# Kernel tuning notes

Measured on AMD Instinct MI355X. Metric: run time of the kernel, lower is better.

## Reference

```python
import jax, jax.numpy as jnp
import numpy as np

T, KBLK, EMB, B = 2048, 64, 512, 4


def _make_coords(t, k):
    # head1: for each j, cols = block_start(j) + arange(j % k + 1)  (block-causal local)
    j = np.arange(t)
    cnt1 = (j % k) + 1
    rows1 = np.repeat(j, cnt1)
    off1 = np.arange(cnt1.sum()) - np.repeat(np.cumsum(cnt1) - cnt1, cnt1)
    cols1 = (rows1 // k) * k + off1
    # head2: for each block start c, rows = arange(c, t), col = c  (strided block-start)
    starts = np.arange(t // k) * k
    cnt2 = t - starts
    base = np.repeat(starts, cnt2)
    off2 = np.arange(cnt2.sum()) - np.repeat(np.cumsum(cnt2) - cnt2, cnt2)
    rows2, cols2 = base + off2, base
    c1 = np.stack([rows1, cols1], 1).astype(np.int32)
    c2 = np.stack([rows2, cols2], 1).astype(np.int32)
    return c1, c2


def setup_inputs() -> dict:
    key = jax.random.key(0)
    ks = jax.random.split(key, 6)
    s = 1.0 / float(np.sqrt(EMB))
    c1, c2 = _make_coords(T, KBLK)
    return {
        "x": jax.random.normal(ks[0], (B, T, EMB), jnp.float32),
        "Wk": jax.random.normal(ks[1], (EMB, EMB), jnp.float32) * s,
        "bk": jnp.zeros((EMB,), jnp.float32),
        "Wq": jax.random.normal(ks[2], (EMB, EMB), jnp.float32) * s,
        "bq": jnp.zeros((EMB,), jnp.float32),
        "Wv": jax.random.normal(ks[3], (EMB, EMB), jnp.float32) * s,
        "bv": jnp.zeros((EMB,), jnp.float32),
        "Wu": jax.random.normal(ks[4], (EMB, 2 * EMB), jnp.float32) * s,
        "bu": jnp.zeros((EMB,), jnp.float32),
        "coords1": jnp.asarray(c1),
        "coords2": jnp.asarray(c2),
    }


def _sparse_head(Kt, Qt, Vt, coords):
    rows, cols = coords[:, 0], coords[:, 1]
    # dot[b,p] = (K @ Q^T)[b, rows[p], cols[p]] = K[b,rows[p],:] . Q[b,cols[p],:]
    dot = jnp.einsum('bpe,bpe->bp', Kt[:, rows], Qt[:, cols])
    # sparse.batchmm: out[b,r] = sum_{p: rows[p]=r} dot[b,p] * V[b, cols[p]]
    out = jnp.zeros_like(Vt).at[:, rows].add(dot[..., None] * Vt[:, cols])
    return out


def reference(x, Wk, bk, Wq, bq, Wv, bv, Wu, bu, coords1, coords2):
    Kt = x @ Wk.T + bk
    Qt = x @ Wq.T + bq
    Vt = x @ Wv.T + bv
    h1 = _sparse_head(Kt, Qt, Vt, coords1)
    h2 = _sparse_head(Kt, Qt, Vt, coords2)
    comb = jnp.concatenate([h1, h2], axis=-1)  # [B, T, 2*EMB]
    return comb @ Wu.T + bu
```

## Files before the change

### kernel.cpp

```cpp
#include <hip/hip_runtime.h>


typedef unsigned short u16;
typedef __attribute__((ext_vector_type(8))) short short8;
typedef __attribute__((ext_vector_type(4))) float f32x4;

constexpr int TDIM  = 2048;
constexpr int EMB_D = 512;
constexpr int BB    = 4;
constexpr int NBLK  = 32;
constexpr int LDK   = 2048;

__device__ __forceinline__ u16 f2b(float f) {
    unsigned u = __float_as_uint(f);
    unsigned r = (u + 0x7FFFu + ((u >> 16) & 1u)) >> 16;
    return (u16)r;
}

__global__ __launch_bounds__(256) void prep_k(
    const float* __restrict__ x, const float* __restrict__ Wk, const float* __restrict__ Wq,
    const float* __restrict__ Wv, const float* __restrict__ Wu,
    const float* __restrict__ bk, const float* __restrict__ bq, const float* __restrict__ bv,
    u16* __restrict__ xb, u16* __restrict__ wcat, float* __restrict__ biascat)
{
    const int bid = blockIdx.x, tid = threadIdx.x;
    if (bid < 32) {
        const int bm = (bid >> 2) * 128;
        const int bn = (bid & 3) * 128;
        const int wid  = tid >> 6;
        const int lane = tid & 63;
        const int l15  = lane & 15;
        const int quad = lane >> 4;
        const int wm = (wid & 1) * 64;
        const int wn = (wid >> 1) * 64;

        f32x4 acc[4][4] = {};

        const float* Arow[4];
        #pragma unroll
        for (int i = 0; i < 4; ++i) {
            const int m = bm + wm + 16 * i + l15;
            Arow[i] = Wu + (size_t)(m & 511) * 1024 + (m >> 9) * 512 + quad * 8;
        }
        const float* Bcol[4];
        #pragma unroll
        for (int g = 0; g < 4; ++g)
            Bcol[g] = Wv + (bn + wn + 16 * g + l15) + (size_t)(quad * 8) * 512;

        for (int j0 = 0; j0 < 512; j0 += 32) {
            short8 a[4], b[4];
            #pragma unroll
            for (int i = 0; i < 4; ++i) {
                float4 v0 = *(const float4*)(Arow[i] + j0);
                float4 v1 = *(const float4*)(Arow[i] + j0 + 4);
                a[i] = (short8){(short)f2b(v0.x), (short)f2b(v0.y), (short)f2b(v0.z), (short)f2b(v0.w),
                                (short)f2b(v1.x), (short)f2b(v1.y), (short)f2b(v1.z), (short)f2b(v1.w)};
            }
            #pragma unroll
            for (int g = 0; g < 4; ++g) {
                const float* p = Bcol[g] + (size_t)j0 * 512;
                float v0 = p[0];          float v1 = p[512];
                float v2 = p[1024];       float v3 = p[1536];
                float v4 = p[2048];       float v5 = p[2560];
                float v6 = p[3072];       float v7 = p[3584];
                b[g] = (short8){(short)f2b(v0), (short)f2b(v1), (short)f2b(v2), (short)f2b(v3),
                                (short)f2b(v4), (short)f2b(v5), (short)f2b(v6), (short)f2b(v7)};
            }
            #pragma unroll
            for (int i = 0; i < 4; ++i)
                #pragma unroll
                for (int g = 0; g < 4; ++g)
                    acc[i][g] = __builtin_amdgcn_mfma_f32_16x16x32_bf16(a[i], b[g], acc[i][g], 0, 0, 0);
        }

        #pragma unroll
        for (int i = 0; i < 4; ++i)
            #pragma unroll
            for (int g = 0; g < 4; ++g) {
                const int col = bn + wn + 16 * g + l15;
                #pragma unroll
                for (int r = 0; r < 4; ++r) {
                    const int row = bm + wm + 16 * i + quad * 4 + r;
                    wcat[(size_t)(1024 + row) * 512 + col] = f2b(acc[i][g][r]);
                }
            }
    } else if (bid < 4640) {
        const float* src; u16* dst; int base;
        if (bid < 4128)      { src = x;  dst = xb;            base = (bid - 32) * 1024; }
        else if (bid < 4384) { src = Wk; dst = wcat;          base = (bid - 4128) * 1024; }
        else                 { src = Wq; dst = wcat + 262144; base = (bid - 4384) * 1024; }
        const int idx = base + tid * 4;
        float4 v = *(const float4*)(src + idx);
        ushort4 o = { f2b(v.x), f2b(v.y), f2b(v.z), f2b(v.w) };
        *(ushort4*)(dst + idx) = o;
    } else if (bid < 4656) {
        const int o = (bid - 4640) * 64 + (tid >> 2);
        const int p = tid & 3;
        const int n = o & 511, half = o >> 9;
        const float* wr = Wu + (size_t)n * 1024 + half * 512 + p * 128;
        const float* br = bv + p * 128;
        float s = 0.f;
        #pragma unroll
        for (int j = 0; j < 128; j += 4) {
            float4 a = *(const float4*)(wr + j);
            float4 b = *(const float4*)(br + j);
            s += a.x*b.x + a.y*b.y + a.z*b.z + a.w*b.w;
        }
        s += __shfl_xor(s, 1);
        s += __shfl_xor(s, 2);
        if (p == 0) biascat[1024 + o] = s;
    } else {
        const int idx = tid * 4;
        float4 v = (idx < 512) ? *(const float4*)(bk + idx)
                               : *(const float4*)(bq + idx - 512);
        *(float4*)(biascat + idx) = v;
    }
}

template<int MH, int KK>
__device__ __forceinline__ void mm16(const short8 (&a)[4], const short8 (&b)[2][4],
                                     f32x4 (&acc)[8][4])
{
    #pragma unroll
    for (int f = 0; f < 4; ++f)
        #pragma unroll
        for (int g = 0; g < 4; ++g)
            acc[MH * 4 + f][g] = __builtin_amdgcn_mfma_f32_16x16x32_bf16(
                a[f], b[KK][g], acc[MH * 4 + f][g], 0, 0, 0);
}

template<int SLOT, int MH>
__device__ __forceinline__ void lda4(short8 (&a)[4], const u16* sm, int arow, int koff)
{
    #pragma unroll
    for (int f = 0; f < 4; ++f)
        a[f] = *(const short8*)(sm + SLOT * 32768 + (arow + MH * 64 + f * 16) * 64 + koff);
}

template<int SLOT>
__device__ __forceinline__ void ldb4(short8 (&bk)[4], const u16* sm, int brow, int koff)
{
    #pragma unroll
    for (int g = 0; g < 4; ++g)
        bk[g] = *(const short8*)(sm + SLOT * 32768 + 16384 + (brow + g * 16) * 64 + koff);
}

#define STA(S, CI, T) __builtin_amdgcn_global_load_lds( \
    (const __attribute__((address_space(1))) void*)(Ag + (size_t)(CI) * 32768 + (T) * 64), \
    (__attribute__((address_space(3))) void*)(sm + (S) * 32768 + (CI) * 4096 + wid * 512), 16, 0, 0)
#define STB(S, CI, T) __builtin_amdgcn_global_load_lds( \
    (const __attribute__((address_space(1))) void*)(Bg + (size_t)(CI) * 32768 + (T) * 64), \
    (__attribute__((address_space(3))) void*)(sm + (S) * 32768 + 16384 + (CI) * 4096 + wid * 512), 16, 0, 0)
#define KBAR()  __builtin_amdgcn_s_barrier()
#define KPRIO(P) __builtin_amdgcn_s_setprio(P)
#define LGKM0() do { asm volatile("s_waitcnt lgkmcnt(0)" ::: "memory"); \
                     __builtin_amdgcn_sched_barrier(0); } while (0)
#define VMC4()  asm volatile("s_waitcnt vmcnt(4)" ::: "memory")
#define VMC0()  asm volatile("s_waitcnt vmcnt(0)" ::: "memory")

__global__ __launch_bounds__(512, 2) void kqv_gemm_k(
    const u16* __restrict__ A, const u16* __restrict__ W,
    const float* __restrict__ bias, u16* __restrict__ C)
{
    __shared__ u16 sm[65536];

    const int bid = blockIdx.x;
    const int wg  = (bid & 7) * 32 + (bid >> 3);
    const int bm  = (wg & 31) * 256;
    const int bn  = (wg >> 5) * 256;
    const int tid  = threadIdx.x;
    const int wid  = tid >> 6;
    const int lane = tid & 63;
    const int l15  = lane & 15;
    const int quad = lane >> 4;
    const int wm = wid >> 2;
    const int wn = wid & 3;

    const int stgrow = wid * 8 + (lane >> 3);
    const int stgk   = ((lane & 7) ^ ((lane >> 3) & 7)) << 3;
    const u16* Ag = A + (size_t)(bm + stgrow) * 512 + stgk;
    const u16* Bg = W + (size_t)(bn + stgrow) * 512 + stgk;

    const int r7     = l15 & 7;
    const int arow   = wm * 128 + l15;
    const int brow   = wn * 64 + l15;
    const int off_k0 = ((quad ^ r7) << 3);
    const int off_k1 = (((4 | quad) ^ r7) << 3);

    f32x4 acc[8][4] = {};
    short8 a[4], b[2][4];

    STA(0,0,0); STA(0,2,0); STB(0,0,0); STB(0,1,0);
    STB(0,2,0); STB(0,3,0); STA(0,1,0); STA(0,3,0);
    STA(1,0,1); STA(1,2,1); STB(1,0,1); STB(1,1,1);
    VMC4(); KBAR();

    for (int it = 0; it < 3; ++it) {
        const int t = 2 * it;
        ldb4<0>(b[0], sm, brow, off_k0); lda4<0,0>(a, sm, arow, off_k0);
        STB(1,2,t+1); STB(1,3,t+1);
        KBAR(); LGKM0(); KPRIO(1); mm16<0,0>(a, b, acc); KPRIO(0); KBAR();
        ldb4<0>(b[1], sm, brow, off_k1); lda4<0,0>(a, sm, arow, off_k1);
        STA(1,1,t+1); STA(1,3,t+1);
        KBAR(); LGKM0(); KPRIO(1); mm16<0,1>(a, b, acc); KPRIO(0); KBAR();
        lda4<0,1>(a, sm, arow, off_k0);
        STA(0,0,t+2); STA(0,2,t+2);
        KBAR(); LGKM0(); KPRIO(1); mm16<1,0>(a, b, acc); KPRIO(0); KBAR();
        lda4<0,1>(a, sm, arow, off_k1);
        STB(0,0,t+2); STB(0,1,t+2);
        KBAR(); LGKM0(); KPRIO(1); mm16<1,1>(a, b, acc); KPRIO(0); VMC4(); KBAR();
        ldb4<1>(b[0], sm, brow, off_k0); lda4<1,0>(a, sm, arow, off_k0);
        STB(0,2,t+2); STB(0,3,t+2);
        KBAR(); LGKM0(); KPRIO(1); mm16<0,0>(a, b, acc); KPRIO(0); KBAR();
        ldb4<1>(b[1], sm, brow, off_k1); lda4<1,0>(a, sm, arow, off_k1);
        STA(0,1,t+2); STA(0,3,t+2);
        KBAR(); LGKM0(); KPRIO(1); mm16<0,1>(a, b, acc); KPRIO(0); KBAR();
        lda4<1,1>(a, sm, arow, off_k0);
        STA(1,0,t+3); STA(1,2,t+3);
        KBAR(); LGKM0(); KPRIO(1); mm16<1,0>(a, b, acc); KPRIO(0); KBAR();
        lda4<1,1>(a, sm, arow, off_k1);
        STB(1,0,t+3); STB(1,1,t+3);
        KBAR(); LGKM0(); KPRIO(1); mm16<1,1>(a, b, acc); KPRIO(0); VMC4(); KBAR();
    }

    ldb4<0>(b[0], sm, brow, off_k0); lda4<0,0>(a, sm, arow, off_k0);
    STB(1,2,7); STB(1,3,7);
    KBAR(); LGKM0(); KPRIO(1); mm16<0,0>(a, b, acc); KPRIO(0); KBAR();
    ldb4<0>(b[1], sm, brow, off_k1); lda4<0,0>(a, sm, arow, off_k1);
    STA(1,1,7); STA(1,3,7);
    KBAR(); LGKM0(); KPRIO(1); mm16<0,1>(a, b, acc); KPRIO(0); KBAR();
    lda4<0,1>(a, sm, arow, off_k0);
    KBAR(); LGKM0(); KPRIO(1); mm16<1,0>(a, b, acc); KPRIO(0); KBAR();
    lda4<0,1>(a, sm, arow, off_k1);
    KBAR(); LGKM0(); KPRIO(1); mm16<1,1>(a, b, acc); KPRIO(0); VMC0(); KBAR();
    ldb4<1>(b[0], sm, brow, off_k0); lda4<1,0>(a, sm, arow, off_k0);
    KBAR(); LGKM0(); KPRIO(1); mm16<0,0>(a, b, acc); KPRIO(0); KBAR();
    ldb4<1>(b[1], sm, brow, off_k1); lda4<1,0>(a, sm, arow, off_k1);
    KBAR(); LGKM0(); KPRIO(1); mm16<0,1>(a, b, acc); KPRIO(0); KBAR();
    lda4<1,1>(a, sm, arow, off_k0);
    KBAR(); LGKM0(); KPRIO(1); mm16<1,0>(a, b, acc); KPRIO(0); KBAR();
    lda4<1,1>(a, sm, arow, off_k1);
    KBAR(); LGKM0(); KPRIO(1); mm16<1,1>(a, b, acc); KPRIO(0);

    __syncthreads();
    #pragma unroll
    for (int mf = 0; mf < 8; ++mf) {
        #pragma unroll
        for (int g = 0; g < 4; ++g) {
            const int col = wn * 64 + g * 16 + l15;
            const float bvv = bias[bn + col];
            #pragma unroll
            for (int r = 0; r < 4; ++r) {
                const int row = wm * 128 + mf * 16 + quad * 4 + r;
                sm[row * 256 + col] = f2b(acc[mf][g][r] + bvv);
            }
        }
    }
    __syncthreads();
    {
        const int rr = tid >> 5;
        const int ck = tid & 31;
        #pragma unroll
        for (int p = 0; p < 16; ++p) {
            const int row = p * 16 + rr;
            short8 v = *(const short8*)(sm + row * 256 + ck * 8);
            *(short8*)(C + (size_t)(bm + row) * LDK + bn + ck * 8) = v;
        }
    }
}

#undef STA
#undef STB
#undef KBAR
#undef KPRIO
#undef LGKM0
#undef VMC4
#undef VMC0

__global__ __launch_bounds__(512) void heads_k(
    const u16* __restrict__ KQV, const float* __restrict__ bu, float* __restrict__ out)
{
    __shared__ u16 smA[64 * 104];
    __shared__ u16 smVT[256 * 104];
    __shared__ u16 pK[2][64 * 32];
    __shared__ u16 pQ[2][64 * 32];
    __shared__ u16 pQs[2][32 * 32];

    const int blk = blockIdx.x, b = blockIdx.y;
    const int e0 = blockIdx.z * 256;
    const int tid = threadIdx.x;
    const int wid = tid >> 6, lane = tid & 63;
    const int l15 = lane & 15, quad = lane >> 4;
    const int rw = wid & 3, ch = wid >> 2;
    const size_t row0 = (size_t)b * TDIM + (size_t)blk * 64;
    const size_t brow = (size_t)b * TDIM;
    const int srow_base = 16 * rw + quad * 4;

    #pragma unroll
    for (int it = 0; it < 4; ++it) {
        const int id = tid + 512 * it;
        const int c  = id & 63;
        const int eo = (id >> 6) * 8;
        short8 v = *(const short8*)(KQV + (row0 + c) * (size_t)LDK + 1024 + e0 + eo);
        #pragma unroll
        for (int i = 0; i < 8; ++i) smVT[(eo + i) * 104 + c] = (u16)v[i];
    }
    #pragma unroll
    for (int it = 0; it < 2; ++it) {
        const int id = tid + 512 * it;
        const int m  = id & 31;
        const int eo = (id >> 5) * 8;
        short8 v = *(const short8*)(KQV + (brow + 64 * m) * (size_t)LDK + 1536 + e0 + eo);
        #pragma unroll
        for (int i = 0; i < 8; ++i) smVT[(eo + i) * 104 + 64 + m] = (u16)v[i];
    }

    f32x4 s1[2] = {}; f32x4 s2 = {};
    const int strow  = (tid >> 2) & 63;
    const int sthalf = tid >> 8;
    const int stk    = (tid & 3) * 8;
    const u16* Kg = KQV + (row0 + strow) * (size_t)LDK + sthalf * 32 + stk;
    const u16* Qg = Kg + 512;
    const int qrow  = (tid >> 2) & 31;
    const int qhalf = (tid >> 7) & 1;
    const u16* Qsg = KQV + (brow + (size_t)64 * qrow) * (size_t)LDK + 512 + qhalf * 32 + stk;
    char* dK  = (char*)pK  + wid * 1024;
    char* dQ  = (char*)pQ  + wid * 1024;
    char* dQs = (char*)pQs + wid * 1024;

    for (int k0 = 0; k0 < 512; k0 += 64) {
        __syncthreads();
        __builtin_amdgcn_global_load_lds(
            (const __attribute__((address_space(1))) void*)(Kg + k0),
            (__attribute__((address_space(3))) void*)dK, 16, 0, 0);
        __builtin_amdgcn_global_load_lds(
            (const __attribute__((address_space(1))) void*)(Qg + k0),
            (__attribute__((address_space(3))) void*)dQ, 16, 0, 0);
        if (wid < 4)
            __builtin_amdgcn_global_load_lds(
                (const __attribute__((address_space(1))) void*)(Qsg + k0),
                (__attribute__((address_space(3))) void*)dQs, 16, 0, 0);
        __syncthreads();

        short8 a0 = *(const short8*)(pK[0] + (16 * rw + l15) * 32 + quad * 8);
        short8 a1 = *(const short8*)(pK[1] + (16 * rw + l15) * 32 + quad * 8);
        #pragma unroll
        for (int jj = 0; jj < 2; ++jj) {
            const int j = 2 * ch + jj;
            short8 b0 = *(const short8*)(pQ[0] + (16 * j + l15) * 32 + quad * 8);
            short8 b1 = *(const short8*)(pQ[1] + (16 * j + l15) * 32 + quad * 8);
            s1[jj] = __builtin_amdgcn_mfma_f32_16x16x32_bf16(a0, b0, s1[jj], 0, 0, 0);
            s1[jj] = __builtin_amdgcn_mfma_f32_16x16x32_bf16(a1, b1, s1[jj], 0, 0, 0);
        }
        {
            short8 b0 = *(const short8*)(pQs[0] + (16 * ch + l15) * 32 + quad * 8);
            short8 b1 = *(const short8*)(pQs[1] + (16 * ch + l15) * 32 + quad * 8);
            s2 = __builtin_amdgcn_mfma_f32_16x16x32_bf16(a0, b0, s2, 0, 0, 0);
            s2 = __builtin_amdgcn_mfma_f32_16x16x32_bf16(a1, b1, s2, 0, 0, 0);
        }
    }

    #pragma unroll
    for (int jj = 0; jj < 2; ++jj)
        #pragma unroll
        for (int r = 0; r < 4; ++r) {
            const int rr = srow_base + r;
            const int cc = 32 * ch + 16 * jj + l15;
            smA[rr * 104 + cc] = f2b((cc <= rr) ? s1[jj][r] : 0.0f);
        }
    #pragma unroll
    for (int r = 0; r < 4; ++r) {
        const int m  = 16 * ch + l15;
        const int rr = srow_base + r;
        smA[rr * 104 + 64 + m] = f2b((m <= blk) ? s2[r] : 0.0f);
    }
    __syncthreads();

    f32x4 o[8] = {};
    const u16* arow = smA + (16 * rw + l15) * 104;
    #pragma unroll
    for (int ks = 0; ks < 3; ++ks) {
        short8 as = *(const short8*)(arow + 32 * ks + quad * 8);
        #pragma unroll
        for (int nt = 0; nt < 8; ++nt) {
            short8 bs = *(const short8*)(smVT + (16 * (8 * ch + nt) + l15) * 104 + 32 * ks + quad * 8);
            o[nt] = __builtin_amdgcn_mfma_f32_16x16x32_bf16(as, bs, o[nt], 0, 0, 0);
        }
    }
    #pragma unroll
    for (int nt = 0; nt < 8; ++nt) {
        const int col = e0 + 16 * (8 * ch + nt) + l15;
        const float bvv = bu[col];
        #pragma unroll
        for (int r = 0; r < 4; ++r)
            out[(row0 + srow_base + r) * (size_t)EMB_D + col] = o[nt][r] + bvv;
    }
}

extern "C" void kernel_launch(void* const* d_in, const int* in_sizes, int n_in,
                              void* d_out, int out_size, void* d_ws, size_t ws_size,
                              hipStream_t stream)
{
    const float* x  = (const float*)d_in[0];
    const float* Wk = (const float*)d_in[1];
    const float* bk = (const float*)d_in[2];
    const float* Wq = (const float*)d_in[3];
    const float* bq = (const float*)d_in[4];
    const float* Wv = (const float*)d_in[5];
    const float* bv = (const float*)d_in[6];
    const float* Wu = (const float*)d_in[7];
    const float* bu = (const float*)d_in[8];
    float* out = (float*)d_out;

    char* w = (char*)d_ws;
    u16*   KQV     = (u16*)  (w + ((size_t)0  << 20));
    u16*   xb      = (u16*)  (w + ((size_t)32 << 20));
    u16*   wcat    = (u16*)  (w + ((size_t)40 << 20));
    float* biascat = (float*)(w + ((size_t)44 << 20));

    hipLaunchKernelGGL(prep_k, dim3(4657), dim3(256), 0, stream,
                       x, Wk, Wq, Wv, Wu, bk, bq, bv, xb, wcat, biascat);
    hipLaunchKernelGGL(kqv_gemm_k, dim3(256), dim3(512), 0, stream, xb, wcat, biascat, KQV);
    hipLaunchKernelGGL(heads_k, dim3(NBLK, BB, 2), dim3(512), 0, stream, KQV, bu, out);
}
```

Baseline: 141.5 us.

## Replace pipelined 256x256 GEMM with simple single-buffered 128x256 tiles at higher occupancy

The hand-scheduled, double-buffered 256x256 KQV GEMM with setprio and manual waitcnts is replaced by a plain loop over 128x256 tiles. Each iteration loads one K-slice into LDS and syncs twice, and the grid doubles to 512 blocks. The smaller LDS footprint and accumulator set allow more blocks per CU, and the epilogue now writes bf16 directly to global memory instead of staging through LDS. The cost is the loss of load/compute overlap and more B-matrix traffic. The scattered 2-byte global stores may also hurt coalescing.

```diff
diff --git a/kernel.cpp b/kernel.cpp
--- a/kernel.cpp
+++ b/kernel.cpp
@@ -117,57 +117,15 @@
     }
 }
 
-template<int MH, int KK>
-__device__ __forceinline__ void mm16(const short8 (&a)[4], const short8 (&b)[2][4],
-                                     f32x4 (&acc)[8][4])
-{
-    #pragma unroll
-    for (int f = 0; f < 4; ++f)
-        #pragma unroll
-        for (int g = 0; g < 4; ++g)
-            acc[MH * 4 + f][g] = __builtin_amdgcn_mfma_f32_16x16x32_bf16(
-                a[f], b[KK][g], acc[MH * 4 + f][g], 0, 0, 0);
-}
-
-template<int SLOT, int MH>
-__device__ __forceinline__ void lda4(short8 (&a)[4], const u16* sm, int arow, int koff)
-{
-    #pragma unroll
-    for (int f = 0; f < 4; ++f)
-        a[f] = *(const short8*)(sm + SLOT * 32768 + (arow + MH * 64 + f * 16) * 64 + koff);
-}
-
-template<int SLOT>
-__device__ __forceinline__ void ldb4(short8 (&bk)[4], const u16* sm, int brow, int koff)
-{
-    #pragma unroll
-    for (int g = 0; g < 4; ++g)
-        bk[g] = *(const short8*)(sm + SLOT * 32768 + 16384 + (brow + g * 16) * 64 + koff);
-}
-
-#define STA(S, CI, T) __builtin_amdgcn_global_load_lds( \
-    (const __attribute__((address_space(1))) void*)(Ag + (size_t)(CI) * 32768 + (T) * 64), \
-    (__attribute__((address_space(3))) void*)(sm + (S) * 32768 + (CI) * 4096 + wid * 512), 16, 0, 0)
-#define STB(S, CI, T) __builtin_amdgcn_global_load_lds( \
-    (const __attribute__((address_space(1))) void*)(Bg + (size_t)(CI) * 32768 + (T) * 64), \
-    (__attribute__((address_space(3))) void*)(sm + (S) * 32768 + 16384 + (CI) * 4096 + wid * 512), 16, 0, 0)
-#define KBAR()  __builtin_amdgcn_s_barrier()
-#define KPRIO(P) __builtin_amdgcn_s_setprio(P)
-#define LGKM0() do { asm volatile("s_waitcnt lgkmcnt(0)" ::: "memory"); \
-                     __builtin_amdgcn_sched_barrier(0); } while (0)
-#define VMC4()  asm volatile("s_waitcnt vmcnt(4)" ::: "memory")
-#define VMC0()  asm volatile("s_waitcnt vmcnt(0)" ::: "memory")
-
-__global__ __launch_bounds__(512, 2) void kqv_gemm_k(
+__global__ __launch_bounds__(512, 4) void kqv_gemm_k(
     const u16* __restrict__ A, const u16* __restrict__ W,
     const float* __restrict__ bias, u16* __restrict__ C)
 {
-    __shared__ u16 sm[65536];
+    __shared__ u16 sm[24576];
 
     const int bid = blockIdx.x;
-    const int wg  = (bid & 7) * 32 + (bid >> 3);
-    const int bm  = (wg & 31) * 256;
-    const int bn  = (wg >> 5) * 256;
+    const int bn  = (bid & 7) * 256;
+    const int bm  = (bid >> 3) * 128;
     const int tid  = threadIdx.x;
     const int wid  = tid >> 6;
     const int lane = tid & 63;
@@ -182,100 +140,73 @@
     const u16* Bg = W + (size_t)(bn + stgrow) * 512 + stgk;
 
     const int r7     = l15 & 7;
-    const int arow   = wm * 128 + l15;
-    const int brow   = wn * 64 + l15;
     const int off_k0 = ((quad ^ r7) << 3);
     const int off_k1 = (((4 | quad) ^ r7) << 3);
-
-    f32x4 acc[8][4] = {};
-    short8 a[4], b[2][4];
-
-    STA(0,0,0); STA(0,2,0); STB(0,0,0); STB(0,1,0);
-    STB(0,2,0); STB(0,3,0); STA(0,1,0); STA(0,3,0);
-    STA(1,0,1); STA(1,2,1); STB(1,0,1); STB(1,1,1);
-    VMC4(); KBAR();
-
-    for (int it = 0; it < 3; ++it) {
-        const int t = 2 * it;
-        ldb4<0>(b[0], sm, brow, off_k0); lda4<0,0>(a, sm, arow, off_k0);
-        STB(1,2,t+1); STB(1,3,t+1);
-        KBAR(); LGKM0(); KPRIO(1); mm16<0,0>(a, b, acc); KPRIO(0); KBAR();
-        ldb4<0>(b[1], sm, brow, off_k1); lda4<0,0>(a, sm, arow, off_k1);
-        STA(1,1,t+1); STA(1,3,t+1);
-        KBAR(); LGKM0(); KPRIO(1); mm16<0,1>(a, b, acc); KPRIO(0); KBAR();
-        lda4<0,1>(a, sm, arow, off_k0);
-        STA(0,0,t+2); STA(0,2,t+2);
-        KBAR(); LGKM0(); KPRIO(1); mm16<1,0>(a, b, acc); KPRIO(0); KBAR();
-        lda4<0,1>(a, sm, arow, off_k1);
-        STB(0,0,t+2); STB(0,1,t+2);
-        KBAR(); LGKM0(); KPRIO(1); mm16<1,1>(a, b, acc); KPRIO(0); VMC4(); KBAR();
-        ldb4<1>(b[0], sm, brow, off_k0); lda4<1,0>(a, sm, arow, off_k0);
-        STB(0,2,t+2); STB(0,3,t+2);
-        KBAR(); LGKM0(); KPRIO(1); mm16<0,0>(a, b, acc); KPRIO(0); KBAR();
-        ldb4<1>(b[1], sm, brow, off_k1); lda4<1,0>(a, sm, arow, off_k1);
-        STA(0,1,t+2); STA(0,3,t+2);
-        KBAR(); LGKM0(); KPRIO(1); mm16<0,1>(a, b, acc); KPRIO(0); KBAR();
-        lda4<1,1>(a, sm, arow, off_k0);
-        STA(1,0,t+3); STA(1,2,t+3);
-        KBAR(); LGKM0(); KPRIO(1); mm16<1,0>(a, b, acc); KPRIO(0); KBAR();
-        lda4<1,1>(a, sm, arow, off_k1);
-        STB(1,0,t+3); STB(1,1,t+3);
-        KBAR(); LGKM0(); KPRIO(1); mm16<1,1>(a, b, acc); KPRIO(0); VMC4(); KBAR();
-    }
-
-    ldb4<0>(b[0], sm, brow, off_k0); lda4<0,0>(a, sm, arow, off_k0);
-    STB(1,2,7); STB(1,3,7);
-    KBAR(); LGKM0(); KPRIO(1); mm16<0,0>(a, b, acc); KPRIO(0); KBAR();
-    ldb4<0>(b[1], sm, brow, off_k1); lda4<0,0>(a, sm, arow, off_k1);
-    STA(1,1,7); STA(1,3,7);
-    KBAR(); LGKM0(); KPRIO(1); mm16<0,1>(a, b, acc); KPRIO(0); KBAR();
-    lda4<0,1>(a, sm, arow, off_k0);
-    KBAR(); LGKM0(); KPRIO(1); mm16<1,0>(a, b, acc); KPRIO(0); KBAR();
-    lda4<0,1>(a, sm, arow, off_k1);
-    KBAR(); LGKM0(); KPRIO(1); mm16<1,1>(a, b, acc); KPRIO(0); VMC0(); KBAR();
-    ldb4<1>(b[0], sm, brow, off_k0); lda4<1,0>(a, sm, arow, off_k0);
-    KBAR(); LGKM0(); KPRIO(1); mm16<0,0>(a, b, acc); KPRIO(0); KBAR();
-    ldb4<1>(b[1], sm, brow, off_k1); lda4<1,0>(a, sm, arow, off_k1);
-    KBAR(); LGKM0(); KPRIO(1); mm16<0,1>(a, b, acc); KPRIO(0); KBAR();
-    lda4<1,1>(a, sm, arow, off_k0);
-    KBAR(); LGKM0(); KPRIO(1); mm16<1,0>(a, b, acc); KPRIO(0); KBAR();
-    lda4<1,1>(a, sm, arow, off_k1);
-    KBAR(); LGKM0(); KPRIO(1); mm16<1,1>(a, b, acc); KPRIO(0);
-
-    __syncthreads();
-    #pragma unroll
-    for (int mf = 0; mf < 8; ++mf) {
+    const int arow0  = wm * 64 + l15;
+    const int brow0  = wn * 64 + l15;
+
+    f32x4 acc[4][4] = {};
+
+    for (int t = 0; t < 8; ++t) {
+        __syncthreads();
+        const int tk = t * 64;
+        __builtin_amdgcn_global_load_lds(
+            (const __attribute__((address_space(1))) void*)(Ag + tk),
+            (__attribute__((address_space(3))) void*)(sm + wid * 512), 16, 0, 0);
+        __builtin_amdgcn_global_load_lds(
+            (const __attribute__((address_space(1))) void*)(Ag + 32768 + tk),
+            (__attribute__((address_space(3))) void*)(sm + 4096 + wid * 512), 16, 0, 0);
+        #pragma unroll
+        for (int c = 0; c < 4; ++c)
+            __builtin_amdgcn_global_load_lds(
+                (const __attribute__((address_space(1))) void*)(Bg + (size_t)c * 32768 + tk),
+                (__attribute__((address_space(3))) void*)(sm + 8192 + c * 4096 + wid * 512), 16, 0, 0);
+        __syncthreads();
+
+        {
+            short8 a[4], b[4];
+            #pragma unroll
+            for (int f = 0; f < 4; ++f)
+                a[f] = *(const short8*)(sm + (arow0 + f * 16) * 64 + off_k0);
+            #pragma unroll
+            for (int g = 0; g < 4; ++g)
+                b[g] = *(const short8*)(sm + 8192 + (brow0 + g * 16) * 64 + off_k0);
+            #pragma unroll
+            for (int f = 0; f < 4; ++f)
+                #pragma unroll
+                for (int g = 0; g < 4; ++g)
+                    acc[f][g] = __builtin_amdgcn_mfma_f32_16x16x32_bf16(a[f], b[g], acc[f][g], 0, 0, 0);
+        }
+        {
+            short8 a[4], b[4];
+            #pragma unroll
+            for (int f = 0; f < 4; ++f)
+                a[f] = *(const short8*)(sm + (arow0 + f * 16) * 64 + off_k1);
+            #pragma unroll
+            for (int g = 0; g < 4; ++g)
+                b[g] = *(const short8*)(sm + 8192 + (brow0 + g * 16) * 64 + off_k1);
+            #pragma unroll
+            for (int f = 0; f < 4; ++f)
+                #pragma unroll
+                for (int g = 0; g < 4; ++g)
+                    acc[f][g] = __builtin_amdgcn_mfma_f32_16x16x32_bf16(a[f], b[g], acc[f][g], 0, 0, 0);
+        }
+    }
+
+    #pragma unroll
+    for (int f = 0; f < 4; ++f) {
         #pragma unroll
         for (int g = 0; g < 4; ++g) {
-            const int col = wn * 64 + g * 16 + l15;
-            const float bvv = bias[bn + col];
+            const int col = bn + wn * 64 + g * 16 + l15;
+            const float bvv = bias[col];
             #pragma unroll
             for (int r = 0; r < 4; ++r) {
-                const int row = wm * 128 + mf * 16 + quad * 4 + r;
-                sm[row * 256 + col] = f2b(acc[mf][g][r] + bvv);
+                const int row = bm + wm * 64 + f * 16 + quad * 4 + r;
+                C[(size_t)row * LDK + col] = f2b(acc[f][g][r] + bvv);
             }
         }
     }
-    __syncthreads();
-    {
-        const int rr = tid >> 5;
-        const int ck = tid & 31;
-        #pragma unroll
-        for (int p = 0; p < 16; ++p) {
-            const int row = p * 16 + rr;
-            short8 v = *(const short8*)(sm + row * 256 + ck * 8);
-            *(short8*)(C + (size_t)(bm + row) * LDK + bn + ck * 8) = v;
-        }
-    }
-}
-
-#undef STA
-#undef STB
-#undef KBAR
-#undef KPRIO
-#undef LGKM0
-#undef VMC4
-#undef VMC0
+}
 
 __global__ __launch_bounds__(512) void heads_k(
     const u16* __restrict__ KQV, const float* __restrict__ bu, float* __restrict__ out)
@@ -420,6 +351,6 @@
 
     hipLaunchKernelGGL(prep_k, dim3(4657), dim3(256), 0, stream,
                        x, Wk, Wq, Wv, Wu, bk, bq, bv, xb, wcat, biascat);
-    hipLaunchKernelGGL(kqv_gemm_k, dim3(256), dim3(512), 0, stream, xb, wcat, biascat, KQV);
+    hipLaunchKernelGGL(kqv_gemm_k, dim3(512), dim3(512), 0, stream, xb, wcat, biascat, KQV);
     hipLaunchKernelGGL(heads_k, dim3(NBLK, BB, 2), dim3(512), 0, stream, KQV, bu, out);
 }
```

Measured after the change: 147.3 us. 1.04x slower.

## Triple-buffer K/Q staging in heads kernel and overlap V transpose loads

Applied to the files above, without the earlier changes.

Replaces the double-synchronized single-stage K/Q/Qs load loop in heads_k with a three-buffer pipeline that prefetches two k-tiles ahead, using explicit vmcnt waits and raw barriers instead of full __syncthreads. The V-tile global loads are now issued up front into registers, and their transposed LDS writes happen after the first stages are in flight, hiding global latency behind the transpose. This uses more LDS (three staging buffers) and relies on hand-counted vmcnt values that must match the per-wave number of outstanding loads.

```diff
diff --git a/kernel.cpp b/kernel.cpp
--- a/kernel.cpp
+++ b/kernel.cpp
@@ -271,20 +271,22 @@
 
 #undef STA
 #undef STB
-#undef KBAR
-#undef KPRIO
 #undef LGKM0
 #undef VMC4
 #undef VMC0
 
+#define HVW(N) asm volatile("s_waitcnt vmcnt(" #N ")" ::: "memory")
+#define HAS1 __attribute__((address_space(1)))
+#define HAS3 __attribute__((address_space(3)))
+
 __global__ __launch_bounds__(512) void heads_k(
     const u16* __restrict__ KQV, const float* __restrict__ bu, float* __restrict__ out)
 {
     __shared__ u16 smA[64 * 104];
     __shared__ u16 smVT[256 * 104];
-    __shared__ u16 pK[2][64 * 32];
-    __shared__ u16 pQ[2][64 * 32];
-    __shared__ u16 pQs[2][32 * 32];
+    __shared__ u16 pK[3][4096];
+    __shared__ u16 pQ[3][4096];
+    __shared__ u16 pQs[3][2048];
 
     const int blk = blockIdx.x, b = blockIdx.y;
     const int e0 = blockIdx.z * 256;
@@ -292,30 +294,28 @@
     const int wid = tid >> 6, lane = tid & 63;
     const int l15 = lane & 15, quad = lane >> 4;
     const int rw = wid & 3, ch = wid >> 2;
+    const int uwid = __builtin_amdgcn_readfirstlane(wid);
     const size_t row0 = (size_t)b * TDIM + (size_t)blk * 64;
     const size_t brow = (size_t)b * TDIM;
     const int srow_base = 16 * rw + quad * 4;
 
+    short8 vu1[4]; short8 vu2[2];
+    int vc1[4], ve1[4], vm2[2], ve2[2];
     #pragma unroll
     for (int it = 0; it < 4; ++it) {
         const int id = tid + 512 * it;
-        const int c  = id & 63;
-        const int eo = (id >> 6) * 8;
-        short8 v = *(const short8*)(KQV + (row0 + c) * (size_t)LDK + 1024 + e0 + eo);
-        #pragma unroll
-        for (int i = 0; i < 8; ++i) smVT[(eo + i) * 104 + c] = (u16)v[i];
+        vc1[it] = id & 63;
+        ve1[it] = (id >> 6) * 8;
+        vu1[it] = *(const short8*)(KQV + (row0 + vc1[it]) * (size_t)LDK + 1024 + e0 + ve1[it]);
     }
     #pragma unroll
     for (int it = 0; it < 2; ++it) {
         const int id = tid + 512 * it;
-        const int m  = id & 31;
-        const int eo = (id >> 5) * 8;
-        short8 v = *(const short8*)(KQV + (brow + 64 * m) * (size_t)LDK + 1536 + e0 + eo);
-        #pragma unroll
-        for (int i = 0; i < 8; ++i) smVT[(eo + i) * 104 + 64 + m] = (u16)v[i];
-    }
-
-    f32x4 s1[2] = {}; f32x4 s2 = {};
+        vm2[it] = id & 31;
+        ve2[it] = (id >> 5) * 8;
+        vu2[it] = *(const short8*)(KQV + (brow + 64 * vm2[it]) * (size_t)LDK + 1536 + e0 + ve2[it]);
+    }
+
     const int strow  = (tid >> 2) & 63;
     const int sthalf = tid >> 8;
     const int stk    = (tid & 3) * 8;
@@ -324,41 +324,61 @@
     const int qrow  = (tid >> 2) & 31;
     const int qhalf = (tid >> 7) & 1;
     const u16* Qsg = KQV + (brow + (size_t)64 * qrow) * (size_t)LDK + 512 + qhalf * 32 + stk;
-    char* dK  = (char*)pK  + wid * 1024;
-    char* dQ  = (char*)pQ  + wid * 1024;
-    char* dQs = (char*)pQs + wid * 1024;
-
-    for (int k0 = 0; k0 < 512; k0 += 64) {
-        __syncthreads();
-        __builtin_amdgcn_global_load_lds(
-            (const __attribute__((address_space(1))) void*)(Kg + k0),
-            (__attribute__((address_space(3))) void*)dK, 16, 0, 0);
-        __builtin_amdgcn_global_load_lds(
-            (const __attribute__((address_space(1))) void*)(Qg + k0),
-            (__attribute__((address_space(3))) void*)dQ, 16, 0, 0);
-        if (wid < 4)
-            __builtin_amdgcn_global_load_lds(
-                (const __attribute__((address_space(1))) void*)(Qsg + k0),
-                (__attribute__((address_space(3))) void*)dQs, 16, 0, 0);
-        __syncthreads();
-
-        short8 a0 = *(const short8*)(pK[0] + (16 * rw + l15) * 32 + quad * 8);
-        short8 a1 = *(const short8*)(pK[1] + (16 * rw + l15) * 32 + quad * 8);
+
+#define HSTAGE(BUF, T) do { \
+    __builtin_amdgcn_global_load_lds((const HAS1 void*)(Kg + (T) * 64), \
+        (HAS3 void*)((char*)pK + (BUF) * 8192 + wid * 1024), 16, 0, 0); \
+    __builtin_amdgcn_global_load_lds((const HAS1 void*)(Qg + (T) * 64), \
+        (HAS3 void*)((char*)pQ + (BUF) * 8192 + wid * 1024), 16, 0, 0); \
+    if (wid < 4) \
+        __builtin_amdgcn_global_load_lds((const HAS1 void*)(Qsg + (T) * 64), \
+            (HAS3 void*)((char*)pQs + (BUF) * 4096 + wid * 1024), 16, 0, 0); \
+} while (0)
+
+    HSTAGE(0, 0);
+    HSTAGE(1, 1);
+
+    #pragma unroll
+    for (int it = 0; it < 4; ++it)
+        #pragma unroll
+        for (int i = 0; i < 8; ++i) smVT[(ve1[it] + i) * 104 + vc1[it]] = (u16)vu1[it][i];
+    #pragma unroll
+    for (int it = 0; it < 2; ++it)
+        #pragma unroll
+        for (int i = 0; i < 8; ++i) smVT[(ve2[it] + i) * 104 + 64 + vm2[it]] = (u16)vu2[it][i];
+
+    f32x4 s1[2] = {}; f32x4 s2 = {};
+    #pragma unroll
+    for (int t = 0; t < 8; ++t) {
+        if (t < 6) HSTAGE((t + 2) % 3, t + 2);
+        if (t < 6)       { if (uwid < 4) HVW(6); else HVW(4); }
+        else if (t == 6) { if (uwid < 4) HVW(3); else HVW(2); }
+        else             { HVW(0); }
+        __builtin_amdgcn_sched_barrier(0);
+        __builtin_amdgcn_s_barrier();
+
+        const u16* bK  = pK[t % 3];
+        const u16* bQ  = pQ[t % 3];
+        const u16* bQs = pQs[t % 3];
+        short8 a0 = *(const short8*)(bK + (16 * rw + l15) * 32 + quad * 8);
+        short8 a1 = *(const short8*)(bK + 2048 + (16 * rw + l15) * 32 + quad * 8);
         #pragma unroll
         for (int jj = 0; jj < 2; ++jj) {
             const int j = 2 * ch + jj;
-            short8 b0 = *(const short8*)(pQ[0] + (16 * j + l15) * 32 + quad * 8);
-            short8 b1 = *(const short8*)(pQ[1] + (16 * j + l15) * 32 + quad * 8);
+            short8 b0 = *(const short8*)(bQ + (16 * j + l15) * 32 + quad * 8);
+            short8 b1 = *(const short8*)(bQ + 2048 + (16 * j + l15) * 32 + quad * 8);
             s1[jj] = __builtin_amdgcn_mfma_f32_16x16x32_bf16(a0, b0, s1[jj], 0, 0, 0);
             s1[jj] = __builtin_amdgcn_mfma_f32_16x16x32_bf16(a1, b1, s1[jj], 0, 0, 0);
         }
         {
-            short8 b0 = *(const short8*)(pQs[0] + (16 * ch + l15) * 32 + quad * 8);
-            short8 b1 = *(const short8*)(pQs[1] + (16 * ch + l15) * 32 + quad * 8);
+            short8 b0 = *(const short8*)(bQs + (16 * ch + l15) * 32 + quad * 8);
+            short8 b1 = *(const short8*)(bQs + 1024 + (16 * ch + l15) * 32 + quad * 8);
             s2 = __builtin_amdgcn_mfma_f32_16x16x32_bf16(a0, b0, s2, 0, 0, 0);
             s2 = __builtin_amdgcn_mfma_f32_16x16x32_bf16(a1, b1, s2, 0, 0, 0);
         }
-    }
+        __builtin_amdgcn_s_barrier();
+    }
+#undef HSTAGE
 
     #pragma unroll
     for (int jj = 0; jj < 2; ++jj)
```

Measured after the change: 142.1 us. About the same (+0.4%).
